# Optimization experiments

Hardware: AMD Instinct MI355X
Metric: run time of the kernel (lower is better)

Reference implementation:

```python
import jax, jax.numpy as jnp
import numpy as np

G, C, L, D, H, NCLS = 64, 32, 128, 64, 128, 10


def setup_inputs() -> dict:
    key = jax.random.key(0)
    ks = jax.random.split(key, 5)
    scale = 0.05
    return {
        "cycle_reps": jax.random.normal(ks[0], (G, C, L, D), dtype=jnp.float32),
        "W_ih": jax.random.normal(ks[1], (4 * H, D), dtype=jnp.float32) * scale,
        "W_hh": jax.random.normal(ks[2], (4 * H, H), dtype=jnp.float32) * scale,
        "b_ih": jnp.zeros((4 * H,), dtype=jnp.float32),
        "b_hh": jnp.zeros((4 * H,), dtype=jnp.float32),
        "W_cls": jax.random.normal(ks[3], (NCLS, H), dtype=jnp.float32) * scale,
        "b_cls": jnp.zeros((NCLS,), dtype=jnp.float32),
    }


def _lstm_seq_sum(x, W_ih, W_hh, b):
    """Run a single-layer LSTM over x [B, L, D]; return sum of hidden states over L -> [B, H]."""
    B = x.shape[0]
    Hh = W_hh.shape[1]
    # precompute input-side gate pre-activations for all timesteps: [L, B, 4H]
    xg = jnp.einsum('bld,gd->lbg', x, W_ih) + b

    def step(carry, xg_t):
        h, c = carry
        gates = xg_t + h @ W_hh.T  # [B, 4H]
        i, f, g, o = jnp.split(gates, 4, axis=-1)  # torch i/f/g/o gate order
        i = jax.nn.sigmoid(i)
        f = jax.nn.sigmoid(f)
        g = jnp.tanh(g)
        o = jax.nn.sigmoid(o)
        c = f * c + i * g
        h = o * jnp.tanh(c)
        return (h, c), h

    init = (jnp.zeros((B, Hh), x.dtype), jnp.zeros((B, Hh), x.dtype))
    _, hs = jax.lax.scan(step, init, xg)  # hs: [L, B, H]
    return hs.sum(axis=0)


def reference(cycle_reps, W_ih, W_hh, b_ih, b_hh, W_cls, b_cls):
    Gn, Cn, Ln, Dn = cycle_reps.shape
    x = cycle_reps.reshape(Gn * Cn, Ln, Dn)
    rep = _lstm_seq_sum(x, W_ih, W_hh, b_ih + b_hh)  # [G*C, H]: sum of LSTM outputs over seq
    rep = rep.reshape(Gn, Cn, -1)
    # torch.var_mean over the cycle axis; only the mean is used as the graph rep
    graph_mean = rep.mean(axis=1)  # [G, H]
    logits = graph_mean @ W_cls.T + b_cls  # classifier_gnn
    return jax.nn.log_softmax(logits, axis=1)
```

## Files before the change

kernel.cpp:

```cpp
#include <hip/hip_runtime.h>
#include <hip/hip_bf16.h>

#define NSEQ 2048
#define LSEQ 128
#define DIN  64
#define HID  128
#define NCLS 10
#define XPAD 72
#define CHK  16

typedef __attribute__((ext_vector_type(8))) short bfrag8;
typedef __attribute__((ext_vector_type(4))) float facc4;

__device__ __forceinline__ short f2bf(float f) {
    union { __hip_bfloat16 b; short s; } u;
    u.b = __float2bfloat16(f);
    return u.s;
}

__device__ __forceinline__ bfrag8 load_bf16_frag(const float* __restrict__ p) {
    bfrag8 r;
#pragma unroll
    for (int j = 0; j < 8; ++j) r[j] = f2bf(p[j]);
    return r;
}

__device__ __forceinline__ float fast_sigmoid(float x) {
    float e = __builtin_amdgcn_exp2f(-1.4426950408889634f * x);
    return __builtin_amdgcn_rcpf(1.0f + e);
}
__device__ __forceinline__ float fast_tanh(float x) {
    float e = __builtin_amdgcn_exp2f(2.8853900817779268f * x);
    return 1.0f - 2.0f * __builtin_amdgcn_rcpf(1.0f + e);
}

__device__ __forceinline__ float lane_redistribute(float r_low, float r_high) {
    float d = r_low, s = r_high;
    asm("v_permlane32_swap_b32 %0, %1" : "+v"(d), "+v"(s));
    return d;
}

__global__ __launch_bounds__(512) void lstm_fused(
    const float* __restrict__ x,
    const float* __restrict__ Wih,
    const float* __restrict__ Whh,
    const float* __restrict__ bih,
    const float* __restrict__ bhh,
    float* __restrict__ rep)
{
    __shared__ __align__(16) __hip_bfloat16 hbuf[2][16][136];
    __shared__ __align__(16) __hip_bfloat16 xs[2][CHK][8][XPAD];

    const int tid  = threadIdx.x;
    const int w    = tid >> 6;
    const int lane = tid & 63;
    const int ln   = lane & 15;
    const int qd   = lane >> 4;
    const int s0   = blockIdx.x * 8;
    const int khid = w * 16 + ln;
    const int sq0  = (qd & 1) * 4 + (qd >> 1) * 2;
    const int sq1  = sq0 + 1;

    bfrag8 whh[4][4];
    bfrag8 wih[4][2];
    facc4  biasf[4];
#pragma unroll
    for (int g = 0; g < 4; ++g) {
        const int col = g * HID + khid;
        const float b = bih[col] + bhh[col];
        biasf[g] = (facc4){b, b, b, b};
#pragma unroll
        for (int k0 = 0; k0 < 4; ++k0)
            whh[g][k0] = load_bf16_frag(Whh + col * HID + k0 * 32 + qd * 8);
#pragma unroll
        for (int k0 = 0; k0 < 2; ++k0)
            wih[g][k0] = load_bf16_frag(Wih + col * DIN + k0 * 32 + qd * 8);
    }

    {
        unsigned int* p = (unsigned int*)&hbuf[0][0][0];
        for (int i = tid; i < 2 * 16 * 136 / 2; i += 512) p[i] = 0u;
    }

    const float* xsrc = x + (size_t)(s0 + w) * (LSEQ * DIN) + lane * 16;
    const int stt = lane >> 2;
    const int sdd = (lane & 3) * 16;

    {
        float4 a0 = ((const float4*)xsrc)[0];
        float4 a1 = ((const float4*)xsrc)[1];
        float4 a2 = ((const float4*)xsrc)[2];
        float4 a3 = ((const float4*)xsrc)[3];
        bfrag8 o0, o1;
#pragma unroll
        for (int j = 0; j < 4; ++j) { o0[j] = f2bf(((float*)&a0)[j]); o0[4+j] = f2bf(((float*)&a1)[j]); }
#pragma unroll
        for (int j = 0; j < 4; ++j) { o1[j] = f2bf(((float*)&a2)[j]); o1[4+j] = f2bf(((float*)&a3)[j]); }
        *(bfrag8*)&xs[0][stt][w][sdd]     = o0;
        *(bfrag8*)&xs[0][stt][w][sdd + 8] = o1;
    }

    float cst[2]  = {0.f, 0.f};
    float hsum[2] = {0.f, 0.f};

    __syncthreads();

    facc4 accA[4], accB[4];
    {
        bfrag8 x0 = *(const bfrag8*)(&xs[0][0][ln & 7][qd * 8]);
        bfrag8 x1 = *(const bfrag8*)(&xs[0][0][ln & 7][32 + qd * 8]);
#pragma unroll
        for (int g = 0; g < 4; ++g) {
            accA[g] = __builtin_amdgcn_mfma_f32_16x16x32_bf16(x0, wih[g][0], biasf[g], 0, 0, 0);
            accA[g] = __builtin_amdgcn_mfma_f32_16x16x32_bf16(x1, wih[g][1], accA[g], 0, 0, 0);
        }
    }

    int cur = 0;

#define STEP(ACCIN, ACCOUT, CT)                                                          \
    {                                                                                    \
        const int ct = (CT);                                                             \
                                             \
        bfrag8 hf[4];                                                                    \
        _Pragma("unroll")                                                                \
        for (int k0 = 0; k0 < 4; ++k0)                                                   \
            hf[k0] = *(const bfrag8*)(&hbuf[cur][ln][k0 * 32 + qd * 8]);                 \
             \
        const int nbuf = (ct < CHK - 1) ? buf : (buf ^ 1);                               \
        const int nct  = (ct + 1) & (CHK - 1);                                           \
        bfrag8 xf0 = *(const bfrag8*)(&xs[nbuf][nct][ln & 7][qd * 8]);                   \
        bfrag8 xf1 = *(const bfrag8*)(&xs[nbuf][nct][ln & 7][32 + qd * 8]);              \
                    \
        _Pragma("unroll")                                                                \
        for (int g = 0; g < 4; ++g)                                                      \
            _Pragma("unroll")                                                            \
            for (int k0 = 0; k0 < 4; ++k0)                                               \
                ACCIN[g] = __builtin_amdgcn_mfma_f32_16x16x32_bf16(hf[k0], whh[g][k0], ACCIN[g], 0, 0, 0); \
                        \
        float u0[4], u1[4];                                                              \
        _Pragma("unroll")                                                                \
        for (int g = 0; g < 4; ++g) {                                                    \
            u0[g] = lane_redistribute(ACCIN[g][0], ACCIN[g][2]);                         \
            u1[g] = lane_redistribute(ACCIN[g][1], ACCIN[g][3]);                         \
        }                                                                                \
                  \
        _Pragma("unroll")                                                                \
        for (int g = 0; g < 4; ++g) {                                                    \
            ACCOUT[g] = __builtin_amdgcn_mfma_f32_16x16x32_bf16(xf0, wih[g][0], biasf[g], 0, 0, 0); \
            ACCOUT[g] = __builtin_amdgcn_mfma_f32_16x16x32_bf16(xf1, wih[g][1], ACCOUT[g], 0, 0, 0); \
        }                                                                                \
        if (ct == 0 && more) {                      \
            const float* p = xsrc + (chunk + 1) * (CHK * DIN);                           \
            l0 = ((const float4*)p)[0];                                                  \
            l1 = ((const float4*)p)[1];                                                  \
            l2 = ((const float4*)p)[2];                                                  \
            l3 = ((const float4*)p)[3];                                                  \
        }                                                                                \
        if (ct == 12 && more) {                   \
            bfrag8 o0, o1;                                                               \
            _Pragma("unroll")                                                            \
            for (int j = 0; j < 4; ++j) { o0[j] = f2bf(((float*)&l0)[j]); o0[4+j] = f2bf(((float*)&l1)[j]); } \
            _Pragma("unroll")                                                            \
            for (int j = 0; j < 4; ++j) { o1[j] = f2bf(((float*)&l2)[j]); o1[4+j] = f2bf(((float*)&l3)[j]); } \
            *(bfrag8*)&xs[buf ^ 1][stt][w][sdd]     = o0;                                \
            *(bfrag8*)&xs[buf ^ 1][stt][w][sdd + 8] = o1;                                \
        }                                                                                \
                               \
        short hb[2];                                                                     \
        _Pragma("unroll")                                                                \
        for (int j = 0; j < 2; ++j) {                                                    \
            float iv = fast_sigmoid(j ? u1[0] : u0[0]);                                  \
            float fv = fast_sigmoid(j ? u1[1] : u0[1]);                                  \
            float gv = fast_tanh(j ? u1[2] : u0[2]);                                     \
            float ov = fast_sigmoid(j ? u1[3] : u0[3]);                                  \
            float c  = fv * cst[j] + iv * gv;                                            \
            cst[j]   = c;                                                                \
            float hv = ov * fast_tanh(c);                                                \
            hsum[j] += hv;                                                               \
            hb[j]    = f2bf(hv);                                                         \
        }                                                                                \
        ((short*)&hbuf[cur ^ 1][sq0][0])[khid] = hb[0];                                  \
        ((short*)&hbuf[cur ^ 1][sq1][0])[khid] = hb[1];                                  \
        __syncthreads();                                                                 \
        cur ^= 1;                                                                        \
    }

    for (int chunk = 0; chunk < LSEQ / CHK; ++chunk) {
        const int buf = chunk & 1;
        const bool more = chunk < (LSEQ / CHK - 1);
        float4 l0, l1, l2, l3;
#pragma unroll 1
        for (int ct2 = 0; ct2 < CHK / 2; ++ct2) {
            STEP(accA, accB, 2 * ct2);
            STEP(accB, accA, 2 * ct2 + 1);
        }
    }
#undef STEP

    rep[(size_t)(s0 + sq0) * HID + khid] = hsum[0];
    rep[(size_t)(s0 + sq1) * HID + khid] = hsum[1];
}

__global__ __launch_bounds__(128) void cls_kernel(
    const float* __restrict__ rep,
    const float* __restrict__ Wcls,
    const float* __restrict__ bcls,
    float* __restrict__ out)
{
    __shared__ float m_s[HID];
    __shared__ float logits_s[NCLS];
    const int g = blockIdx.x;
    const int h = threadIdx.x;

    float s = 0.f;
#pragma unroll 4
    for (int c = 0; c < 32; ++c)
        s += rep[((size_t)g * 32 + c) * HID + h];
    m_s[h] = s * (1.0f / 32.0f);
    __syncthreads();

    if (h < NCLS) {
        float acc = bcls[h];
        for (int k = 0; k < HID; ++k)
            acc += m_s[k] * Wcls[h * HID + k];
        logits_s[h] = acc;
    }
    __syncthreads();

    if (h < NCLS) {
        float mx = logits_s[0];
#pragma unroll
        for (int j = 1; j < NCLS; ++j) mx = fmaxf(mx, logits_s[j]);
        float se = 0.f;
#pragma unroll
        for (int j = 0; j < NCLS; ++j)
            se += __builtin_amdgcn_exp2f((logits_s[j] - mx) * 1.4426950408889634f);
        float lse = mx + 0.6931471805599453f * __builtin_amdgcn_logf(se);
        out[g * NCLS + h] = logits_s[h] - lse;
    }
}

extern "C" void kernel_launch(void* const* d_in, const int* in_sizes, int n_in,
                              void* d_out, int out_size, void* d_ws, size_t ws_size,
                              hipStream_t stream) {
    const float* x    = (const float*)d_in[0];
    const float* Wih  = (const float*)d_in[1];
    const float* Whh  = (const float*)d_in[2];
    const float* bih  = (const float*)d_in[3];
    const float* bhh  = (const float*)d_in[4];
    const float* Wcls = (const float*)d_in[5];
    const float* bcls = (const float*)d_in[6];

    float* rep = (float*)d_ws;

    lstm_fused<<<NSEQ / 8, 512, 0, stream>>>(x, Wih, Whh, bih, bhh, rep);
    cls_kernel<<<64, 128, 0, stream>>>(rep, Wcls, bcls, (float*)d_out);
}
```

Before: 200.5 us.

## Split LSTM block into recurrent and input-projection warp groups via LDS ring

Doubles the block to 1024 threads. Eight waves run only the recurrent h@W_hh MFMAs and gate math, and eight producer waves compute the input-side gate pre-activations (x@W_ih + bias) two steps ahead into a triple-buffered fp32 LDS ring. This takes the input projection and the x loads off the recurrent critical path. Recurrent waves raise MFMA priority with s_setprio. The cost is a 1024-wide barrier every timestep, extra LDS traffic for the fp32 gate buffer, and likely one block per CU.

Result: no change. 199.8 us (-0.3%).

```diff
diff --git a/kernel.cpp b/kernel.cpp
--- a/kernel.cpp
+++ b/kernel.cpp
@@ -6,8 +6,6 @@
 #define DIN  64
 #define HID  128
 #define NCLS 10
-#define XPAD 72
-#define CHK  16
 
 typedef __attribute__((ext_vector_type(8))) short bfrag8;
 typedef __attribute__((ext_vector_type(4))) float facc4;
@@ -40,7 +38,7 @@
     return d;
 }
 
-__global__ __launch_bounds__(512) void lstm_fused(
+__global__ __launch_bounds__(1024) void lstm_fused(
     const float* __restrict__ x,
     const float* __restrict__ Wih,
     const float* __restrict__ Whh,
@@ -48,8 +46,9 @@
     const float* __restrict__ bhh,
     float* __restrict__ rep)
 {
-    __shared__ __align__(16) __hip_bfloat16 hbuf[2][16][136];
-    __shared__ __align__(16) __hip_bfloat16 xs[2][CHK][8][XPAD];
+    __shared__ __align__(16) __hip_bfloat16 hbuf[2][8][136];
+    __shared__ __align__(16) float xgbuf[3][512][8];
+    __shared__ __align__(16) __hip_bfloat16 xstage[2][8][72];
 
     const int tid  = threadIdx.x;
     const int w    = tid >> 6;
@@ -57,149 +56,157 @@
     const int ln   = lane & 15;
     const int qd   = lane >> 4;
     const int s0   = blockIdx.x * 8;
-    const int khid = w * 16 + ln;
-    const int sq0  = (qd & 1) * 4 + (qd >> 1) * 2;
-    const int sq1  = sq0 + 1;
-
-    bfrag8 whh[4][4];
-    bfrag8 wih[4][2];
-    facc4  biasf[4];
-#pragma unroll
-    for (int g = 0; g < 4; ++g) {
-        const int col = g * HID + khid;
-        const float b = bih[col] + bhh[col];
-        biasf[g] = (facc4){b, b, b, b};
-#pragma unroll
-        for (int k0 = 0; k0 < 4; ++k0)
-            whh[g][k0] = load_bf16_frag(Whh + col * HID + k0 * 32 + qd * 8);
-#pragma unroll
-        for (int k0 = 0; k0 < 2; ++k0)
-            wih[g][k0] = load_bf16_frag(Wih + col * DIN + k0 * 32 + qd * 8);
+
+    if (w < 8) {
+        const int khid = w * 16 + ln;
+        const int sq0  = (qd & 1) * 4 + (qd >> 1) * 2;
+        const int sq1  = sq0 + 1;
+
+        bfrag8 whr[4][4];
+#pragma unroll
+        for (int g = 0; g < 4; ++g) {
+            const int col = g * HID + khid;
+#pragma unroll
+            for (int k0 = 0; k0 < 4; ++k0)
+                whr[g][k0] = load_bf16_frag(Whh + col * HID + k0 * 32 + qd * 8);
+        }
+
+        {
+            unsigned int* ph = (unsigned int*)&hbuf[0][0][0];
+            for (int i = tid; i < 2 * 8 * 136 / 2; i += 512) ph[i] = 0u;
+        }
+
+        float cst[2]  = {0.f, 0.f};
+        float hsum[2] = {0.f, 0.f};
+
+        __syncthreads();
+
+        const int xoff = khid * 8 + (qd & 1) * 4;
+        facc4 acc[4];
+#pragma unroll
+        for (int g = 0; g < 4; ++g)
+            acc[g] = *(const facc4*)(&xgbuf[0][0][0] + g * 1024 + xoff);
+
+        int cur = 0, bufN = 1;
+#pragma unroll 1
+        for (int t = 0; t < LSEQ; ++t) {
+            bfrag8 hf0 = *(const bfrag8*)(&hbuf[cur][ln & 7][qd * 8]);
+            bfrag8 hf1 = *(const bfrag8*)(&hbuf[cur][ln & 7][32 + qd * 8]);
+            bfrag8 hf2 = *(const bfrag8*)(&hbuf[cur][ln & 7][64 + qd * 8]);
+            bfrag8 hf3 = *(const bfrag8*)(&hbuf[cur][ln & 7][96 + qd * 8]);
+            __builtin_amdgcn_s_setprio(1);
+#pragma unroll
+            for (int g = 0; g < 4; ++g) {
+                acc[g] = __builtin_amdgcn_mfma_f32_16x16x32_bf16(hf0, whr[g][0], acc[g], 0, 0, 0);
+                acc[g] = __builtin_amdgcn_mfma_f32_16x16x32_bf16(hf1, whr[g][1], acc[g], 0, 0, 0);
+                acc[g] = __builtin_amdgcn_mfma_f32_16x16x32_bf16(hf2, whr[g][2], acc[g], 0, 0, 0);
+                acc[g] = __builtin_amdgcn_mfma_f32_16x16x32_bf16(hf3, whr[g][3], acc[g], 0, 0, 0);
+            }
+            __builtin_amdgcn_s_setprio(0);
+
+            float u0[4], u1[4];
+#pragma unroll
+            for (int g = 0; g < 4; ++g) {
+                u0[g] = lane_redistribute(acc[g][0], acc[g][2]);
+                u1[g] = lane_redistribute(acc[g][1], acc[g][3]);
+            }
+
+            {
+                const float* xgN = &xgbuf[bufN][0][0] + xoff;
+#pragma unroll
+                for (int g = 0; g < 4; ++g)
+                    acc[g] = *(const facc4*)(xgN + g * 1024);
+            }
+
+            short hb[2];
+#pragma unroll
+            for (int j = 0; j < 2; ++j) {
+                float iv = fast_sigmoid(j ? u1[0] : u0[0]);
+                float fv = fast_sigmoid(j ? u1[1] : u0[1]);
+                float gv = fast_tanh   (j ? u1[2] : u0[2]);
+                float ov = fast_sigmoid(j ? u1[3] : u0[3]);
+                float c  = fv * cst[j] + iv * gv;
+                cst[j]   = c;
+                float hv = ov * fast_tanh(c);
+                hsum[j] += hv;
+                hb[j]    = f2bf(hv);
+            }
+            ((short*)&hbuf[cur ^ 1][sq0][0])[khid] = hb[0];
+            ((short*)&hbuf[cur ^ 1][sq1][0])[khid] = hb[1];
+
+            __syncthreads();
+            cur ^= 1;
+            bufN = (bufN == 2) ? 0 : bufN + 1;
+        }
+
+        rep[(size_t)(s0 + sq0) * HID + khid] = hsum[0];
+        rep[(size_t)(s0 + sq1) * HID + khid] = hsum[1];
+    } else {
+        const int p = w - 8;
+        const int colbase = p * 16 + ln;
+
+        bfrag8 wir[4][2];
+        facc4  biasf[4];
+#pragma unroll
+        for (int g = 0; g < 4; ++g) {
+            const int col = g * HID + colbase;
+            const float b = bih[col] + bhh[col];
+            biasf[g] = (facc4){b, b, b, b};
+#pragma unroll
+            for (int k0 = 0; k0 < 2; ++k0)
+                wir[g][k0] = load_bf16_frag(Wih + col * DIN + k0 * 32 + qd * 8);
+        }
+
+        const float* xr = x + (size_t)(s0 + (ln & 7)) * (LSEQ * DIN) + qd * 8;
+#pragma unroll
+        for (int tt = 0; tt < 2; ++tt) {
+            float4 a00 = *(const float4*)(xr + tt * DIN);
+            float4 a01 = *(const float4*)(xr + tt * DIN + 4);
+            float4 a10 = *(const float4*)(xr + tt * DIN + 32);
+            float4 a11 = *(const float4*)(xr + tt * DIN + 36);
+            bfrag8 xf0, xf1;
+#pragma unroll
+            for (int j = 0; j < 4; ++j) {
+                xf0[j] = f2bf(((float*)&a00)[j]); xf0[4 + j] = f2bf(((float*)&a01)[j]);
+                xf1[j] = f2bf(((float*)&a10)[j]); xf1[4 + j] = f2bf(((float*)&a11)[j]);
+            }
+#pragma unroll
+            for (int g = 0; g < 4; ++g) {
+                facc4 a = __builtin_amdgcn_mfma_f32_16x16x32_bf16(xf0, wir[g][0], biasf[g], 0, 0, 0);
+                a = __builtin_amdgcn_mfma_f32_16x16x32_bf16(xf1, wir[g][1], a, 0, 0, 0);
+                if (qd < 2)
+                    *(facc4*)(&xgbuf[tt][0][0] + (g * 128 + colbase) * 8 + qd * 4) = a;
+            }
+        }
+
+        const float* xsrow = x + (size_t)(s0 + p) * (LSEQ * DIN) + lane;
+        xstage[0][p][lane] = __float2bfloat16(xsrow[2 * DIN]);
+        float xnext = xsrow[3 * DIN];
+
+        __syncthreads();
+
+        int bufW = 2;
+#pragma unroll 1
+        for (int t = 0; t < LSEQ; ++t) {
+            if (t < LSEQ - 2) {
+                bfrag8 xf0 = *(const bfrag8*)(&xstage[(t + 2) & 1][ln & 7][qd * 8]);
+                bfrag8 xf1 = *(const bfrag8*)(&xstage[(t + 2) & 1][ln & 7][32 + qd * 8]);
+                if (t < LSEQ - 3) {
+                    xstage[(t + 3) & 1][p][lane] = __float2bfloat16(xnext);
+                    if (t < LSEQ - 4) xnext = xsrow[(t + 4) * DIN];
+                }
+#pragma unroll
+                for (int g = 0; g < 4; ++g) {
+                    facc4 a = __builtin_amdgcn_mfma_f32_16x16x32_bf16(xf0, wir[g][0], biasf[g], 0, 0, 0);
+                    a = __builtin_amdgcn_mfma_f32_16x16x32_bf16(xf1, wir[g][1], a, 0, 0, 0);
+                    if (qd < 2)
+                        *(facc4*)(&xgbuf[bufW][0][0] + (g * 128 + colbase) * 8 + qd * 4) = a;
+                }
+            }
+            __syncthreads();
+            bufW = (bufW == 2) ? 0 : bufW + 1;
+        }
     }
-
-    {
-        unsigned int* p = (unsigned int*)&hbuf[0][0][0];
-        for (int i = tid; i < 2 * 16 * 136 / 2; i += 512) p[i] = 0u;
-    }
-
-    const float* xsrc = x + (size_t)(s0 + w) * (LSEQ * DIN) + lane * 16;
-    const int stt = lane >> 2;
-    const int sdd = (lane & 3) * 16;
-
-    {
-        float4 a0 = ((const float4*)xsrc)[0];
-        float4 a1 = ((const float4*)xsrc)[1];
-        float4 a2 = ((const float4*)xsrc)[2];
-        float4 a3 = ((const float4*)xsrc)[3];
-        bfrag8 o0, o1;
-#pragma unroll
-        for (int j = 0; j < 4; ++j) { o0[j] = f2bf(((float*)&a0)[j]); o0[4+j] = f2bf(((float*)&a1)[j]); }
-#pragma unroll
-        for (int j = 0; j < 4; ++j) { o1[j] = f2bf(((float*)&a2)[j]); o1[4+j] = f2bf(((float*)&a3)[j]); }
-        *(bfrag8*)&xs[0][stt][w][sdd]     = o0;
-        *(bfrag8*)&xs[0][stt][w][sdd + 8] = o1;
-    }
-
-    float cst[2]  = {0.f, 0.f};
-    float hsum[2] = {0.f, 0.f};
-
-    __syncthreads();
-
-    facc4 accA[4], accB[4];
-    {
-        bfrag8 x0 = *(const bfrag8*)(&xs[0][0][ln & 7][qd * 8]);
-        bfrag8 x1 = *(const bfrag8*)(&xs[0][0][ln & 7][32 + qd * 8]);
-#pragma unroll
-        for (int g = 0; g < 4; ++g) {
-            accA[g] = __builtin_amdgcn_mfma_f32_16x16x32_bf16(x0, wih[g][0], biasf[g], 0, 0, 0);
-            accA[g] = __builtin_amdgcn_mfma_f32_16x16x32_bf16(x1, wih[g][1], accA[g], 0, 0, 0);
-        }
-    }
-
-    int cur = 0;
-
-#define STEP(ACCIN, ACCOUT, CT)                                                          \
-    {                                                                                    \
-        const int ct = (CT);                                                             \
-                                             \
-        bfrag8 hf[4];                                                                    \
-        _Pragma("unroll")                                                                \
-        for (int k0 = 0; k0 < 4; ++k0)                                                   \
-            hf[k0] = *(const bfrag8*)(&hbuf[cur][ln][k0 * 32 + qd * 8]);                 \
-             \
-        const int nbuf = (ct < CHK - 1) ? buf : (buf ^ 1);                               \
-        const int nct  = (ct + 1) & (CHK - 1);                                           \
-        bfrag8 xf0 = *(const bfrag8*)(&xs[nbuf][nct][ln & 7][qd * 8]);                   \
-        bfrag8 xf1 = *(const bfrag8*)(&xs[nbuf][nct][ln & 7][32 + qd * 8]);              \
-                    \
-        _Pragma("unroll")                                                                \
-        for (int g = 0; g < 4; ++g)                                                      \
-            _Pragma("unroll")                                                            \
-            for (int k0 = 0; k0 < 4; ++k0)                                               \
-                ACCIN[g] = __builtin_amdgcn_mfma_f32_16x16x32_bf16(hf[k0], whh[g][k0], ACCIN[g], 0, 0, 0); \
-                        \
-        float u0[4], u1[4];                                                              \
-        _Pragma("unroll")                                                                \
-        for (int g = 0; g < 4; ++g) {                                                    \
-            u0[g] = lane_redistribute(ACCIN[g][0], ACCIN[g][2]);                         \
-            u1[g] = lane_redistribute(ACCIN[g][1], ACCIN[g][3]);                         \
-        }                                                                                \
-                  \
-        _Pragma("unroll")                                                                \
-        for (int g = 0; g < 4; ++g) {                                                    \
-            ACCOUT[g] = __builtin_amdgcn_mfma_f32_16x16x32_bf16(xf0, wih[g][0], biasf[g], 0, 0, 0); \
-            ACCOUT[g] = __builtin_amdgcn_mfma_f32_16x16x32_bf16(xf1, wih[g][1], ACCOUT[g], 0, 0, 0); \
-        }                                                                                \
-        if (ct == 0 && more) {                      \
-            const float* p = xsrc + (chunk + 1) * (CHK * DIN);                           \
-            l0 = ((const float4*)p)[0];                                                  \
-            l1 = ((const float4*)p)[1];                                                  \
-            l2 = ((const float4*)p)[2];                                                  \
-            l3 = ((const float4*)p)[3];                                                  \
-        }                                                                                \
-        if (ct == 12 && more) {                   \
-            bfrag8 o0, o1;                                                               \
-            _Pragma("unroll")                                                            \
-            for (int j = 0; j < 4; ++j) { o0[j] = f2bf(((float*)&l0)[j]); o0[4+j] = f2bf(((float*)&l1)[j]); } \
-            _Pragma("unroll")                                                            \
-            for (int j = 0; j < 4; ++j) { o1[j] = f2bf(((float*)&l2)[j]); o1[4+j] = f2bf(((float*)&l3)[j]); } \
-            *(bfrag8*)&xs[buf ^ 1][stt][w][sdd]     = o0;                                \
-            *(bfrag8*)&xs[buf ^ 1][stt][w][sdd + 8] = o1;                                \
-        }                                                                                \
-                               \
-        short hb[2];                                                                     \
-        _Pragma("unroll")                                                                \
-        for (int j = 0; j < 2; ++j) {                                                    \
-            float iv = fast_sigmoid(j ? u1[0] : u0[0]);                                  \
-            float fv = fast_sigmoid(j ? u1[1] : u0[1]);                                  \
-            float gv = fast_tanh(j ? u1[2] : u0[2]);                                     \
-            float ov = fast_sigmoid(j ? u1[3] : u0[3]);                                  \
-            float c  = fv * cst[j] + iv * gv;                                            \
-            cst[j]   = c;                                                                \
-            float hv = ov * fast_tanh(c);                                                \
-            hsum[j] += hv;                                                               \
-            hb[j]    = f2bf(hv);                                                         \
-        }                                                                                \
-        ((short*)&hbuf[cur ^ 1][sq0][0])[khid] = hb[0];                                  \
-        ((short*)&hbuf[cur ^ 1][sq1][0])[khid] = hb[1];                                  \
-        __syncthreads();                                                                 \
-        cur ^= 1;                                                                        \
-    }
-
-    for (int chunk = 0; chunk < LSEQ / CHK; ++chunk) {
-        const int buf = chunk & 1;
-        const bool more = chunk < (LSEQ / CHK - 1);
-        float4 l0, l1, l2, l3;
-#pragma unroll 1
-        for (int ct2 = 0; ct2 < CHK / 2; ++ct2) {
-            STEP(accA, accB, 2 * ct2);
-            STEP(accB, accA, 2 * ct2 + 1);
-        }
-    }
-#undef STEP
-
-    rep[(size_t)(s0 + sq0) * HID + khid] = hsum[0];
-    rep[(size_t)(s0 + sq1) * HID + khid] = hsum[1];
 }
 
 __global__ __launch_bounds__(128) void cls_kernel(
@@ -254,6 +261,6 @@
 
     float* rep = (float*)d_ws;
 
-    lstm_fused<<<NSEQ / 8, 512, 0, stream>>>(x, Wih, Whh, bih, bhh, rep);
+    lstm_fused<<<NSEQ / 8, 1024, 0, stream>>>(x, Wih, Whh, bih, bhh, rep);
     cls_kernel<<<64, 128, 0, stream>>>(rep, Wcls, bcls, (float*)d_out);
 }
```

## Halve sequences per block to double grid size and drop permlane redistribution

Applied to the files above, without the earlier changes.

Each block now handles 4 sequences instead of 8, which doubles the number of blocks launched. Within each MFMA output, each lane picks its single gate value with a select, replacing the permlane32 swap, and computes one cell state instead of two. The aim is more parallelism across CUs, since 256 blocks may underfill the device, and less per-step elementwise work along the serial recurrence. In exchange, MFMA rows are duplicated (the 16-row tiles now carry only 4 distinct sequences), so the weights are loaded by twice as many blocks and matrix throughput is wasted.

Measured after the change: 261.8 us. 30.6% more time.

```diff
diff --git a/kernel.cpp b/kernel.cpp
--- a/kernel.cpp
+++ b/kernel.cpp
@@ -6,7 +6,9 @@
 #define DIN  64
 #define HID  128
 #define NCLS 10
-#define XPAD 72
+#define SEQB 4
+#define XPAD 80
+#define HPAD 136
 #define CHK  16
 
 typedef __attribute__((ext_vector_type(8))) short bfrag8;
@@ -32,12 +34,6 @@
 __device__ __forceinline__ float fast_tanh(float x) {
     float e = __builtin_amdgcn_exp2f(2.8853900817779268f * x);
     return 1.0f - 2.0f * __builtin_amdgcn_rcpf(1.0f + e);
-}
-
-__device__ __forceinline__ float lane_redistribute(float r_low, float r_high) {
-    float d = r_low, s = r_high;
-    asm("v_permlane32_swap_b32 %0, %1" : "+v"(d), "+v"(s));
-    return d;
 }
 
 __global__ __launch_bounds__(512) void lstm_fused(
@@ -48,18 +44,16 @@
     const float* __restrict__ bhh,
     float* __restrict__ rep)
 {
-    __shared__ __align__(16) __hip_bfloat16 hbuf[2][16][136];
-    __shared__ __align__(16) __hip_bfloat16 xs[2][CHK][8][XPAD];
+    __shared__ __align__(16) __hip_bfloat16 hbuf[2][SEQB][HPAD];
+    __shared__ __align__(16) __hip_bfloat16 xs[2][CHK][SEQB][XPAD];
 
     const int tid  = threadIdx.x;
     const int w    = tid >> 6;
     const int lane = tid & 63;
     const int ln   = lane & 15;
     const int qd   = lane >> 4;
-    const int s0   = blockIdx.x * 8;
+    const int s0   = blockIdx.x * SEQB;
     const int khid = w * 16 + ln;
-    const int sq0  = (qd & 1) * 4 + (qd >> 1) * 2;
-    const int sq1  = sq0 + 1;
 
     bfrag8 whh[4][4];
     bfrag8 wih[4][2];
@@ -79,14 +73,14 @@
 
     {
         unsigned int* p = (unsigned int*)&hbuf[0][0][0];
-        for (int i = tid; i < 2 * 16 * 136 / 2; i += 512) p[i] = 0u;
-    }
-
-    const float* xsrc = x + (size_t)(s0 + w) * (LSEQ * DIN) + lane * 16;
+        for (int i = tid; i < 2 * SEQB * HPAD / 2; i += 512) p[i] = 0u;
+    }
+
+    const float* xsrc = x + (size_t)(s0 + (w & 3)) * (LSEQ * DIN) + lane * 16;
     const int stt = lane >> 2;
     const int sdd = (lane & 3) * 16;
 
-    {
+    if (w < SEQB) {
         float4 a0 = ((const float4*)xsrc)[0];
         float4 a1 = ((const float4*)xsrc)[1];
         float4 a2 = ((const float4*)xsrc)[2];
@@ -100,15 +94,15 @@
         *(bfrag8*)&xs[0][stt][w][sdd + 8] = o1;
     }
 
-    float cst[2]  = {0.f, 0.f};
-    float hsum[2] = {0.f, 0.f};
+    float cst  = 0.f;
+    float hsum = 0.f;
 
     __syncthreads();
 
     facc4 accA[4], accB[4];
     {
-        bfrag8 x0 = *(const bfrag8*)(&xs[0][0][ln & 7][qd * 8]);
-        bfrag8 x1 = *(const bfrag8*)(&xs[0][0][ln & 7][32 + qd * 8]);
+        bfrag8 x0 = *(const bfrag8*)(&xs[0][0][ln & 3][qd * 8]);
+        bfrag8 x1 = *(const bfrag8*)(&xs[0][0][ln & 3][32 + qd * 8]);
 #pragma unroll
         for (int g = 0; g < 4; ++g) {
             accA[g] = __builtin_amdgcn_mfma_f32_16x16x32_bf16(x0, wih[g][0], biasf[g], 0, 0, 0);
@@ -121,28 +115,29 @@
 #define STEP(ACCIN, ACCOUT, CT)                                                          \
     {                                                                                    \
         const int ct = (CT);                                                             \
-                                             \
+                              \
         bfrag8 hf[4];                                                                    \
         _Pragma("unroll")                                                                \
         for (int k0 = 0; k0 < 4; ++k0)                                                   \
-            hf[k0] = *(const bfrag8*)(&hbuf[cur][ln][k0 * 32 + qd * 8]);                 \
+            hf[k0] = *(const bfrag8*)(&hbuf[cur][ln & 3][k0 * 32 + qd * 8]);             \
              \
         const int nbuf = (ct < CHK - 1) ? buf : (buf ^ 1);                               \
         const int nct  = (ct + 1) & (CHK - 1);                                           \
-        bfrag8 xf0 = *(const bfrag8*)(&xs[nbuf][nct][ln & 7][qd * 8]);                   \
-        bfrag8 xf1 = *(const bfrag8*)(&xs[nbuf][nct][ln & 7][32 + qd * 8]);              \
+        bfrag8 xf0 = *(const bfrag8*)(&xs[nbuf][nct][ln & 3][qd * 8]);                   \
+        bfrag8 xf1 = *(const bfrag8*)(&xs[nbuf][nct][ln & 3][32 + qd * 8]);              \
                     \
         _Pragma("unroll")                                                                \
         for (int g = 0; g < 4; ++g)                                                      \
             _Pragma("unroll")                                                            \
             for (int k0 = 0; k0 < 4; ++k0)                                               \
                 ACCIN[g] = __builtin_amdgcn_mfma_f32_16x16x32_bf16(hf[k0], whh[g][k0], ACCIN[g], 0, 0, 0); \
-                        \
-        float u0[4], u1[4];                                                              \
+                \
+        float u[4];                                                                      \
         _Pragma("unroll")                                                                \
         for (int g = 0; g < 4; ++g) {                                                    \
-            u0[g] = lane_redistribute(ACCIN[g][0], ACCIN[g][2]);                         \
-            u1[g] = lane_redistribute(ACCIN[g][1], ACCIN[g][3]);                         \
+            float a01 = (qd & 1) ? ACCIN[g][1] : ACCIN[g][0];                            \
+            float a23 = (qd & 1) ? ACCIN[g][3] : ACCIN[g][2];                            \
+            u[g] = (qd & 2) ? a23 : a01;                                                 \
         }                                                                                \
                   \
         _Pragma("unroll")                                                                \
@@ -150,14 +145,14 @@
             ACCOUT[g] = __builtin_amdgcn_mfma_f32_16x16x32_bf16(xf0, wih[g][0], biasf[g], 0, 0, 0); \
             ACCOUT[g] = __builtin_amdgcn_mfma_f32_16x16x32_bf16(xf1, wih[g][1], ACCOUT[g], 0, 0, 0); \
         }                                                                                \
-        if (ct == 0 && more) {                      \
+        if (ct == 0 && more && w < SEQB) {          \
             const float* p = xsrc + (chunk + 1) * (CHK * DIN);                           \
             l0 = ((const float4*)p)[0];                                                  \
             l1 = ((const float4*)p)[1];                                                  \
             l2 = ((const float4*)p)[2];                                                  \
             l3 = ((const float4*)p)[3];                                                  \
         }                                                                                \
-        if (ct == 12 && more) {                   \
+        if (ct == 12 && more && w < SEQB) {       \
             bfrag8 o0, o1;                                                               \
             _Pragma("unroll")                                                            \
             for (int j = 0; j < 4; ++j) { o0[j] = f2bf(((float*)&l0)[j]); o0[4+j] = f2bf(((float*)&l1)[j]); } \
@@ -166,22 +161,18 @@
             *(bfrag8*)&xs[buf ^ 1][stt][w][sdd]     = o0;                                \
             *(bfrag8*)&xs[buf ^ 1][stt][w][sdd + 8] = o1;                                \
         }                                                                                \
-                               \
-        short hb[2];                                                                     \
-        _Pragma("unroll")                                                                \
-        for (int j = 0; j < 2; ++j) {                                                    \
-            float iv = fast_sigmoid(j ? u1[0] : u0[0]);                                  \
-            float fv = fast_sigmoid(j ? u1[1] : u0[1]);                                  \
-            float gv = fast_tanh(j ? u1[2] : u0[2]);                                     \
-            float ov = fast_sigmoid(j ? u1[3] : u0[3]);                                  \
-            float c  = fv * cst[j] + iv * gv;                                            \
-            cst[j]   = c;                                                                \
+                                    \
+        {                                                                                \
+            float iv = fast_sigmoid(u[0]);                                               \
+            float fv = fast_sigmoid(u[1]);                                               \
+            float gv = fast_tanh(u[2]);                                                  \
+            float ov = fast_sigmoid(u[3]);                                               \
+            float c  = fv * cst + iv * gv;                                               \
+            cst      = c;                                                                \
             float hv = ov * fast_tanh(c);                                                \
-            hsum[j] += hv;                                                               \
-            hb[j]    = f2bf(hv);                                                         \
-        }                                                                                \
-        ((short*)&hbuf[cur ^ 1][sq0][0])[khid] = hb[0];                                  \
-        ((short*)&hbuf[cur ^ 1][sq1][0])[khid] = hb[1];                                  \
+            hsum    += hv;                                                               \
+            ((short*)&hbuf[cur ^ 1][qd][0])[khid] = f2bf(hv);                            \
+        }                                                                                \
         __syncthreads();                                                                 \
         cur ^= 1;                                                                        \
     }
@@ -198,8 +189,7 @@
     }
 #undef STEP
 
-    rep[(size_t)(s0 + sq0) * HID + khid] = hsum[0];
-    rep[(size_t)(s0 + sq1) * HID + khid] = hsum[1];
+    rep[(size_t)(s0 + qd) * HID + khid] = hsum;
 }
 
 __global__ __launch_bounds__(128) void cls_kernel(
@@ -254,6 +244,6 @@
 
     float* rep = (float*)d_ws;
 
-    lstm_fused<<<NSEQ / 8, 512, 0, stream>>>(x, Wih, Whh, bih, bhh, rep);
+    lstm_fused<<<NSEQ / SEQB, 512, 0, stream>>>(x, Wih, Whh, bih, bhh, rep);
     cls_kernel<<<64, 128, 0, stream>>>(rep, Wcls, bcls, (float*)d_out);
 }
```
